# Kernel tuning notes

Hardware: AMD Instinct MI355X
Metric: run time of the kernel (lower is better)

## Reference

```python
import jax, jax.numpy as jnp
import numpy as np

N_IN = 1024
N_OUT = 1024
T, B = 512, 64


def setup_inputs() -> dict:
    key = jax.random.key(0)
    k1, k2, k3, k4, k5 = jax.random.split(key, 5)
    X = jax.random.normal(k1, (T, B, N_IN), dtype=jnp.float32)
    W = jax.random.normal(k2, (N_IN + N_OUT, 4 * N_OUT), dtype=jnp.float32) * 0.02
    b = jax.random.normal(k3, (4 * N_OUT,), dtype=jnp.float32) * 0.02
    y0 = jax.random.normal(k4, (B, N_OUT), dtype=jnp.float32)
    c0 = jax.random.normal(k5, (B, N_OUT), dtype=jnp.float32)
    i = jnp.ones((T, B), dtype=jnp.float32)  # sequence mask
    return {"X": X, "W": W, "b": b, "y0": y0, "c0": c0, "i": i}


def _lstm_low_mem(X, W, b, y0, c0, i):
    H = y0.shape[-1]
    Wx, Wh = W[: X.shape[-1]], W[X.shape[-1]:]
    # precompute input projection for all steps: [T,B,4H]
    Zx = jnp.einsum('tbi,ih->tbh', X, Wx) + b

    def step(carry, inp):
        y_prev, c_prev = carry
        zx_t, m_t = inp
        z = zx_t + y_prev @ Wh  # [B,4H]
        cell_in = jnp.tanh(z[:, :H])
        in_gate = jax.nn.sigmoid(z[:, H:2 * H])
        fgt_gate = jax.nn.sigmoid(z[:, 2 * H:3 * H])
        out_gate = jax.nn.sigmoid(z[:, 3 * H:])
        c = cell_in * in_gate + c_prev * fgt_gate
        y = jnp.tanh(c) * out_gate
        m = m_t[:, None]
        c = m * c + (1.0 - m) * c_prev
        y = m * y
        return (y, c), (y, c)

    (yT, cT), (Y, C) = jax.lax.scan(step, (y0, c0), (Zx, i))
    return Y, C, cT


def reference(X, W, b, y0, c0, i):
    return _lstm_low_mem(X, W, b, y0, c0, i)
```

## Files before the change

### kernel.cpp

```cpp
#include <hip/hip_runtime.h>
#include <cstdint>
#include <cstddef>

#define T_STEPS 512
#define BB 64
#define NIN 1024
#define HB 1024
#define NGC 4096
#define NSCAN 128
#define HC 8
#define WLDH 1032
#define DRING 16

typedef __attribute__((ext_vector_type(8))) short short8;
typedef __attribute__((ext_vector_type(4))) float float4v;
typedef __attribute__((ext_vector_type(2))) float float2v;

__device__ __forceinline__ unsigned short f2bf(float f) {
    union { float f; unsigned u; } v; v.f = f;
    unsigned r = v.u + 0x7fffu + ((v.u >> 16) & 1u);
    return (unsigned short)(r >> 16);
}

union S8U { short8 v; unsigned short u[8]; unsigned w[4]; };

__global__ void __launch_bounds__(256) cvt_y0_kernel(const float* __restrict__ y0,
                                                     unsigned short* __restrict__ yb1) {
    size_t i = ((size_t)blockIdx.x * 256 + threadIdx.x) * 8;
    float4v a = *(const float4v*)(y0 + i);
    float4v b = *(const float4v*)(y0 + i + 4);
    S8U o;
    o.u[0] = f2bf(a[0]); o.u[1] = f2bf(a[1]); o.u[2] = f2bf(a[2]); o.u[3] = f2bf(a[3]);
    o.u[4] = f2bf(b[0]); o.u[5] = f2bf(b[1]); o.u[6] = f2bf(b[2]); o.u[7] = f2bf(b[3]);
    *(short8*)(yb1 + i) = o.v;
}

__global__ void __launch_bounds__(256, 1)
lstm_fused(const float* __restrict__ X, const float* __restrict__ W,
           const float* __restrict__ bias, const float* __restrict__ y0,
           const float* __restrict__ c0, const float* __restrict__ imask,
           float* __restrict__ out, unsigned* __restrict__ prog,
           float* __restrict__ zring)
{
    extern __shared__ char smem[];
    unsigned short* Wl = (unsigned short*)smem;
    float* zl = (float*)(smem + 32 * WLDH * 2);
    float* cl = zl + 64 * 33;
    float* bl = cl + 64 * 8;

    const int bid = blockIdx.x;
    const bool is_scan = bid < NSCAN;
    const int g   = is_scan ? bid : bid - NSCAN;
    const int tid = threadIdx.x;

    {
        const int kbase = is_scan ? NIN : 0;
        for (int task = tid; task < 1024 * 4; task += 256) {
            int k = task >> 2, gt = task & 3;
            const float* src = W + (size_t)(kbase + k) * NGC + (size_t)gt * HB + (size_t)g * HC;
            #pragma unroll
            for (int c = 0; c < 8; ++c)
                Wl[(gt * 8 + c) * WLDH + k] = f2bf(src[c]);
        }
    }
    if (is_scan) {
        if (tid < 32) {
            int gt = tid >> 3, c = tid & 7;
            bl[tid] = bias[gt * HB + g * HC + c];
        }
        for (int p = tid; p < 512; p += 256) {
            int r = p >> 3, c = p & 7;
            cl[r * 8 + c] = c0[(size_t)r * HB + g * HC + c];
        }
    }
    __syncthreads();

    const int w = tid >> 6, l = tid & 63;
    const int m16 = l & 15, q = l >> 4;
    const int arow = w * 16 + m16;
    const int koff = q * 8;
    const unsigned short* wl0 = Wl + (size_t)m16 * WLDH + koff;
    const unsigned short* wl1 = Wl + (size_t)(16 + m16) * WLDH + koff;

    if (!is_scan) {
        unsigned* fslot = prog + NSCAN + g;
        unsigned* sslot = prog + g;
        for (int t = 0; t < T_STEPS; ++t) {
            float4v acc0 = {0.f, 0.f, 0.f, 0.f};
            float4v acc1 = {0.f, 0.f, 0.f, 0.f};
            const float* xs = X + ((size_t)t * BB + arow) * NIN + koff;
            float4v fbv0[4], fbv1[4];
            #pragma unroll
            for (int p = 0; p < 4; ++p) {
                fbv0[p] = *(const float4v*)(xs + p * 32);
                fbv1[p] = *(const float4v*)(xs + p * 32 + 4);
            }
            #pragma unroll
            for (int kb = 0; kb < 32; ++kb) {
                float4v f0 = fbv0[kb & 3], f1 = fbv1[kb & 3];
                if (kb + 4 < 32) {
                    fbv0[kb & 3] = *(const float4v*)(xs + (kb + 4) * 32);
                    fbv1[kb & 3] = *(const float4v*)(xs + (kb + 4) * 32 + 4);
                }
                S8U o;
                o.u[0] = f2bf(f0[0]); o.u[1] = f2bf(f0[1]); o.u[2] = f2bf(f0[2]); o.u[3] = f2bf(f0[3]);
                o.u[4] = f2bf(f1[0]); o.u[5] = f2bf(f1[1]); o.u[6] = f2bf(f1[2]); o.u[7] = f2bf(f1[3]);
                short8 b0 = *(const short8*)(wl0 + kb * 32);
                short8 b1 = *(const short8*)(wl1 + kb * 32);
                acc0 = __builtin_amdgcn_mfma_f32_16x16x32_bf16(o.v, b0, acc0, 0, 0, 0);
                acc1 = __builtin_amdgcn_mfma_f32_16x16x32_bf16(o.v, b1, acc1, 0, 0, 0);
            }
            if (t >= DRING) {
                if (tid == 0) {
                    const unsigned tgt = (unsigned)(t - DRING + 1);
                    unsigned v;
                    while (1) {
                        asm volatile("global_load_dword %0, %1, off sc0 sc1\n\t"
                                     "s_waitcnt vmcnt(0)" : "=v"(v) : "v"(sslot) : "memory");
                        if (v >= tgt) break;
                        __builtin_amdgcn_s_sleep(2);
                    }
                }
                __syncthreads();
            }
            float* zdst = zring + ((size_t)(t % DRING) * NSCAN + g) * 2048;
            #pragma unroll
            for (int i2 = 0; i2 < 4; ++i2) {
                float* p0 = zdst + (size_t)(w * 16 + q * 4 + i2) * 32 + m16;
                asm volatile("global_store_dword %0, %1, off sc0 sc1" :: "v"(p0), "v"(acc0[i2]) : "memory");
                asm volatile("global_store_dword %0, %1, off offset:64 sc0 sc1" :: "v"(p0), "v"(acc1[i2]) : "memory");
            }
            asm volatile("s_waitcnt vmcnt(0)" ::: "memory");
            __syncthreads();
            if (tid == 0) {
                unsigned v = (unsigned)(t + 1);
                asm volatile("global_store_dword %0, %1, off sc0 sc1" :: "v"(fslot), "v"(v) : "memory");
            }
        }
        return;
    }

    float* Yout  = out;
    float* Cout  = out + (size_t)T_STEPS * BB * HB;
    float* cTout = Cout + (size_t)T_STEPS * BB * HB;
    unsigned short* yb0 = (unsigned short*)cTout;
    unsigned short* yb1 = yb0 + BB * HB;

    const int gr = tid >> 2;
    const int gc = (tid & 3) << 1;

    const unsigned* pp0 = prog + l;
    const unsigned* pp1 = prog + 64 + l;
    const unsigned* ppf = prog + NSCAN + g;

    for (int t = 0; t < T_STEPS; ++t) {
        float mrow = imask[(size_t)t * BB + gr];

        if (tid < 64) {
            unsigned a0, a1, ff;
            const unsigned st = (unsigned)t, ft = (unsigned)(t + 1);
            while (1) {
                asm volatile("global_load_dword %0, %1, off sc0 sc1" : "=v"(a0) : "v"(pp0));
                asm volatile("global_load_dword %0, %1, off sc0 sc1" : "=v"(a1) : "v"(pp1));
                asm volatile("global_load_dword %0, %1, off sc0 sc1" : "=v"(ff) : "v"(ppf));
                asm volatile("s_waitcnt vmcnt(0)" ::: "memory");
                bool ok = (a0 >= st) & (a1 >= st) & (ff >= ft);
                if (__ballot(ok) == ~0ull) break;
                __builtin_amdgcn_s_sleep(2);
            }
        }
        __syncthreads();

        const unsigned short* ybr = ((t & 1) ? yb0 : yb1) + (size_t)arow * HB + koff;
        short8 yreg[32];
        #pragma unroll
        for (int kb = 0; kb < 32; ++kb)
            asm volatile("global_load_dwordx4 %0, %1, off offset:%2 sc0 sc1"
                         : "=v"(yreg[kb]) : "v"(ybr), "i"(kb * 64));
        const float* zp = zring + ((size_t)(t % DRING) * NSCAN + g) * 2048 + (size_t)gr * 32 + gc;
        float2v zx0, zx1, zx2, zx3;
        asm volatile("global_load_dwordx2 %0, %1, off sc0 sc1"            : "=v"(zx0) : "v"(zp));
        asm volatile("global_load_dwordx2 %0, %1, off offset:32 sc0 sc1"  : "=v"(zx1) : "v"(zp));
        asm volatile("global_load_dwordx2 %0, %1, off offset:64 sc0 sc1"  : "=v"(zx2) : "v"(zp));
        asm volatile("global_load_dwordx2 %0, %1, off offset:96 sc0 sc1"  : "=v"(zx3) : "v"(zp));

        short8 b0a[4], b1a[4];
        #pragma unroll
        for (int p = 0; p < 4; ++p) {
            b0a[p] = *(const short8*)(wl0 + p * 32);
            b1a[p] = *(const short8*)(wl1 + p * 32);
        }
        asm volatile("s_waitcnt vmcnt(0)" ::: "memory");
        __builtin_amdgcn_sched_barrier(0);

        float4v acc0 = {0.f, 0.f, 0.f, 0.f};
        float4v acc1 = {0.f, 0.f, 0.f, 0.f};
        #pragma unroll
        for (int kb = 0; kb < 32; ++kb) {
            short8 b0 = b0a[kb & 3], b1 = b1a[kb & 3];
            if (kb + 4 < 32) {
                b0a[kb & 3] = *(const short8*)(wl0 + (kb + 4) * 32);
                b1a[kb & 3] = *(const short8*)(wl1 + (kb + 4) * 32);
            }
            acc0 = __builtin_amdgcn_mfma_f32_16x16x32_bf16(yreg[kb], b0, acc0, 0, 0, 0);
            acc1 = __builtin_amdgcn_mfma_f32_16x16x32_bf16(yreg[kb], b1, acc1, 0, 0, 0);
        }

        #pragma unroll
        for (int i2 = 0; i2 < 4; ++i2) {
            int r = w * 16 + q * 4 + i2;
            zl[r * 33 + m16]      = acc0[i2];
            zl[r * 33 + 16 + m16] = acc1[i2];
        }
        __syncthreads();

        if (t == T_STEPS - 1) {
            if (tid == 0) {
                unsigned v = (unsigned)(T_STEPS + 1);
                asm volatile("global_store_dword %0, %1, off sc0 sc1" :: "v"(prog + g), "v"(v) : "memory");
            }
            if (tid < 64) {
                unsigned a0, a1;
                const unsigned st = (unsigned)(T_STEPS + 1);
                while (1) {
                    asm volatile("global_load_dword %0, %1, off sc0 sc1" : "=v"(a0) : "v"(pp0));
                    asm volatile("global_load_dword %0, %1, off sc0 sc1" : "=v"(a1) : "v"(pp1));
                    asm volatile("s_waitcnt vmcnt(0)" ::: "memory");
                    bool ok = (a0 >= st) & (a1 >= st);
                    if (__ballot(ok) == ~0ull) break;
                    __builtin_amdgcn_s_sleep(2);
                }
            }
            __syncthreads();
        }

        {
            const int r = gr, c = gc;
            float z00 = zl[r * 33 + c]      + zx0[0] + bl[c];
            float z01 = zl[r * 33 + c + 1]  + zx0[1] + bl[c + 1];
            float z10 = zl[r * 33 + 8 + c]  + zx1[0] + bl[8 + c];
            float z11 = zl[r * 33 + 9 + c]  + zx1[1] + bl[9 + c];
            float z20 = zl[r * 33 + 16 + c] + zx2[0] + bl[16 + c];
            float z21 = zl[r * 33 + 17 + c] + zx2[1] + bl[17 + c];
            float z30 = zl[r * 33 + 24 + c] + zx3[0] + bl[24 + c];
            float z31 = zl[r * 33 + 25 + c] + zx3[1] + bl[25 + c];
            float cp0 = cl[r * 8 + c], cp1 = cl[r * 8 + c + 1];
            float m = mrow;
            float cell0 = tanhf(z00),                 cell1 = tanhf(z01);
            float ig0 = 1.f / (1.f + __expf(-z10)),   ig1 = 1.f / (1.f + __expf(-z11));
            float fg0 = 1.f / (1.f + __expf(-z20)),   fg1 = 1.f / (1.f + __expf(-z21));
            float og0 = 1.f / (1.f + __expf(-z30)),   og1 = 1.f / (1.f + __expf(-z31));
            float cn0 = cell0 * ig0 + cp0 * fg0,      cn1 = cell1 * ig1 + cp1 * fg1;
            float yn0 = tanhf(cn0) * og0,             yn1 = tanhf(cn1) * og1;
            cn0 = m * cn0 + (1.f - m) * cp0;          cn1 = m * cn1 + (1.f - m) * cp1;
            yn0 *= m;                                 yn1 *= m;
            cl[r * 8 + c] = cn0; cl[r * 8 + c + 1] = cn1;

            if (t < T_STEPS - 1) {
                unsigned short* ybw = ((t & 1) ? yb1 : yb0) + (size_t)r * HB + (size_t)g * HC + c;
                unsigned pk = (unsigned)f2bf(yn0) | ((unsigned)f2bf(yn1) << 16);
                asm volatile("global_store_dword %0, %1, off sc0 sc1" :: "v"(ybw), "v"(pk) : "memory");
                asm volatile("s_waitcnt vmcnt(0)" ::: "memory");
                __syncthreads();
                if (tid == 0) {
                    unsigned v = (unsigned)(t + 1);
                    asm volatile("global_store_dword %0, %1, off sc0 sc1" :: "v"(prog + g), "v"(v) : "memory");
                }
            }

            size_t oidx = ((size_t)t * BB + r) * HB + (size_t)g * HC + c;
            float2v yv = {yn0, yn1}; *(float2v*)(Yout + oidx) = yv;
            float2v cv = {cn0, cn1}; *(float2v*)(Cout + oidx) = cv;
            if (t == T_STEPS - 1) {
                float2v ct = {cn0, cn1};
                *(float2v*)(cTout + (size_t)r * HB + (size_t)g * HC + c) = ct;
            }
        }
    }
}

extern "C" void kernel_launch(void* const* d_in, const int* in_sizes, int n_in,
                              void* d_out, int out_size, void* d_ws, size_t ws_size,
                              hipStream_t stream) {
    const float* X    = (const float*)d_in[0];
    const float* W    = (const float*)d_in[1];
    const float* bias = (const float*)d_in[2];
    const float* y0   = (const float*)d_in[3];
    const float* c0   = (const float*)d_in[4];
    const float* im   = (const float*)d_in[5];
    float* out = (float*)d_out;

    unsigned* prog = (unsigned*)d_ws;
    float* zring   = (float*)((char*)d_ws + 4096);

    unsigned short* yb0 = (unsigned short*)(out + (size_t)2 * T_STEPS * BB * HB);
    unsigned short* yb1 = yb0 + (size_t)BB * HB;

    const int smem_bytes = 32 * WLDH * 2 + 64 * 33 * 4 + 64 * 8 * 4 + 32 * 4;

    hipMemsetAsync(d_ws, 0, 4096, stream);

    cvt_y0_kernel<<<(BB * HB) / (256 * 8), 256, 0, stream>>>(y0, yb1);

    hipFuncSetAttribute((const void*)lstm_fused,
                        hipFuncAttributeMaxDynamicSharedMemorySize, smem_bytes);
    lstm_fused<<<2 * NSCAN, 256, smem_bytes, stream>>>(X, W, bias, y0, c0, im, out, prog, zring);
}
```

Before: 5.337 ms.

## Split recurrent matmul over K across waves with LDS partial-sum reduction

The scan blocks now split the 1024-long K dimension of the recurrent y@Wh product across the four waves, with each wave covering all 64 batch rows over 256 K values, instead of each wave covering 16 rows over the full K. Partial sums go to four separate LDS tiles and are added together in the gate computation. Each wave preloads its weight slice before polling. Each wave now also polls only the 32 producer flags for its own K range, so waiting is spread across the waves and the block-wide barrier before the matmul is dropped. The cost is four times the LDS z-buffer, an extra reduction step, and more registers held live per wave.

```diff
diff --git a/kernel.cpp b/kernel.cpp
--- a/kernel.cpp
+++ b/kernel.cpp
@@ -45,7 +45,7 @@
     extern __shared__ char smem[];
     unsigned short* Wl = (unsigned short*)smem;
     float* zl = (float*)(smem + 32 * WLDH * 2);
-    float* cl = zl + 64 * 33;
+    float* cl = zl + 4 * 64 * 33;
     float* bl = cl + 64 * 8;
 
     const int bid = blockIdx.x;
@@ -77,12 +77,12 @@
 
     const int w = tid >> 6, l = tid & 63;
     const int m16 = l & 15, q = l >> 4;
-    const int arow = w * 16 + m16;
     const int koff = q * 8;
-    const unsigned short* wl0 = Wl + (size_t)m16 * WLDH + koff;
-    const unsigned short* wl1 = Wl + (size_t)(16 + m16) * WLDH + koff;
 
     if (!is_scan) {
+        const unsigned short* wl0 = Wl + (size_t)m16 * WLDH + koff;
+        const unsigned short* wl1 = Wl + (size_t)(16 + m16) * WLDH + koff;
+        const int arow = w * 16 + m16;
         unsigned* fslot = prog + NSCAN + g;
         unsigned* sslot = prog + g;
         for (int t = 0; t < T_STEPS; ++t) {
@@ -146,37 +146,55 @@
     unsigned short* yb0 = (unsigned short*)cTout;
     unsigned short* yb1 = yb0 + BB * HB;
 
+    const int K0 = w * 256;
+    const unsigned short* wlA = Wl + (size_t)m16 * WLDH + K0 + koff;
+    const unsigned short* wlB = Wl + (size_t)(16 + m16) * WLDH + K0 + koff;
+    float* zlw = zl + w * (64 * 33);
+
     const int gr = tid >> 2;
     const int gc = (tid & 3) << 1;
 
+    const unsigned* pollp = prog + 32 * w + (l & 31);
+    const unsigned* ppf   = prog + NSCAN + g;
     const unsigned* pp0 = prog + l;
     const unsigned* pp1 = prog + 64 + l;
-    const unsigned* ppf = prog + NSCAN + g;
 
     for (int t = 0; t < T_STEPS; ++t) {
         float mrow = imask[(size_t)t * BB + gr];
 
-        if (tid < 64) {
-            unsigned a0, a1, ff;
+        short8 bf0[8], bf1[8];
+        #pragma unroll
+        for (int k2 = 0; k2 < 8; ++k2) {
+            bf0[k2] = *(const short8*)(wlA + k2 * 32);
+            bf1[k2] = *(const short8*)(wlB + k2 * 32);
+        }
+
+        {
             const unsigned st = (unsigned)t, ft = (unsigned)(t + 1);
+            unsigned a0, ff;
             while (1) {
-                asm volatile("global_load_dword %0, %1, off sc0 sc1" : "=v"(a0) : "v"(pp0));
-                asm volatile("global_load_dword %0, %1, off sc0 sc1" : "=v"(a1) : "v"(pp1));
+                asm volatile("global_load_dword %0, %1, off sc0 sc1" : "=v"(a0) : "v"(pollp));
                 asm volatile("global_load_dword %0, %1, off sc0 sc1" : "=v"(ff) : "v"(ppf));
                 asm volatile("s_waitcnt vmcnt(0)" ::: "memory");
-                bool ok = (a0 >= st) & (a1 >= st) & (ff >= ft);
+                bool ok = (ff >= ft) && ((l >= 32) || (a0 >= st));
                 if (__ballot(ok) == ~0ull) break;
-                __builtin_amdgcn_s_sleep(2);
-            }
-        }
-        __syncthreads();
-
-        const unsigned short* ybr = ((t & 1) ? yb0 : yb1) + (size_t)arow * HB + koff;
-        short8 yreg[32];
+                __builtin_amdgcn_s_sleep(1);
+            }
+        }
+
+        const unsigned short* ybase = ((t & 1) ? yb0 : yb1);
+        const unsigned short* p0 = ybase + (size_t)m16 * HB + K0 + koff;
+        const unsigned short* p1 = p0 + 16 * HB;
+        const unsigned short* p2 = p0 + 32 * HB;
+        const unsigned short* p3 = p0 + 48 * HB;
+        short8 yA[8], yB[8], yC[8], yD[8];
         #pragma unroll
-        for (int kb = 0; kb < 32; ++kb)
-            asm volatile("global_load_dwordx4 %0, %1, off offset:%2 sc0 sc1"
-                         : "=v"(yreg[kb]) : "v"(ybr), "i"(kb * 64));
+        for (int k2 = 0; k2 < 8; ++k2) {
+            asm volatile("global_load_dwordx4 %0, %1, off offset:%2 sc0 sc1" : "=v"(yA[k2]) : "v"(p0), "i"(k2 * 64));
+            asm volatile("global_load_dwordx4 %0, %1, off offset:%2 sc0 sc1" : "=v"(yB[k2]) : "v"(p1), "i"(k2 * 64));
+            asm volatile("global_load_dwordx4 %0, %1, off offset:%2 sc0 sc1" : "=v"(yC[k2]) : "v"(p2), "i"(k2 * 64));
+            asm volatile("global_load_dwordx4 %0, %1, off offset:%2 sc0 sc1" : "=v"(yD[k2]) : "v"(p3), "i"(k2 * 64));
+        }
         const float* zp = zring + ((size_t)(t % DRING) * NSCAN + g) * 2048 + (size_t)gr * 32 + gc;
         float2v zx0, zx1, zx2, zx3;
         asm volatile("global_load_dwordx2 %0, %1, off sc0 sc1"            : "=v"(zx0) : "v"(zp));
@@ -184,33 +202,36 @@
         asm volatile("global_load_dwordx2 %0, %1, off offset:64 sc0 sc1"  : "=v"(zx2) : "v"(zp));
         asm volatile("global_load_dwordx2 %0, %1, off offset:96 sc0 sc1"  : "=v"(zx3) : "v"(zp));
 
-        short8 b0a[4], b1a[4];
+        asm volatile("s_waitcnt vmcnt(0) lgkmcnt(0)" ::: "memory");
+        __builtin_amdgcn_sched_barrier(0);
+
+        float4v aA0 = {0.f,0.f,0.f,0.f}, aA1 = {0.f,0.f,0.f,0.f};
+        float4v aB0 = {0.f,0.f,0.f,0.f}, aB1 = {0.f,0.f,0.f,0.f};
+        float4v aC0 = {0.f,0.f,0.f,0.f}, aC1 = {0.f,0.f,0.f,0.f};
+        float4v aD0 = {0.f,0.f,0.f,0.f}, aD1 = {0.f,0.f,0.f,0.f};
         #pragma unroll
-        for (int p = 0; p < 4; ++p) {
-            b0a[p] = *(const short8*)(wl0 + p * 32);
-            b1a[p] = *(const short8*)(wl1 + p * 32);
-        }
-        asm volatile("s_waitcnt vmcnt(0)" ::: "memory");
-        __builtin_amdgcn_sched_barrier(0);
-
-        float4v acc0 = {0.f, 0.f, 0.f, 0.f};
-        float4v acc1 = {0.f, 0.f, 0.f, 0.f};
-        #pragma unroll
-        for (int kb = 0; kb < 32; ++kb) {
-            short8 b0 = b0a[kb & 3], b1 = b1a[kb & 3];
-            if (kb + 4 < 32) {
-                b0a[kb & 3] = *(const short8*)(wl0 + (kb + 4) * 32);
-                b1a[kb & 3] = *(const short8*)(wl1 + (kb + 4) * 32);
-            }
-            acc0 = __builtin_amdgcn_mfma_f32_16x16x32_bf16(yreg[kb], b0, acc0, 0, 0, 0);
-            acc1 = __builtin_amdgcn_mfma_f32_16x16x32_bf16(yreg[kb], b1, acc1, 0, 0, 0);
+        for (int k2 = 0; k2 < 8; ++k2) {
+            short8 b0 = bf0[k2], b1 = bf1[k2];
+            aA0 = __builtin_amdgcn_mfma_f32_16x16x32_bf16(yA[k2], b0, aA0, 0, 0, 0);
+            aA1 = __builtin_amdgcn_mfma_f32_16x16x32_bf16(yA[k2], b1, aA1, 0, 0, 0);
+            aB0 = __builtin_amdgcn_mfma_f32_16x16x32_bf16(yB[k2], b0, aB0, 0, 0, 0);
+            aB1 = __builtin_amdgcn_mfma_f32_16x16x32_bf16(yB[k2], b1, aB1, 0, 0, 0);
+            aC0 = __builtin_amdgcn_mfma_f32_16x16x32_bf16(yC[k2], b0, aC0, 0, 0, 0);
+            aC1 = __builtin_amdgcn_mfma_f32_16x16x32_bf16(yC[k2], b1, aC1, 0, 0, 0);
+            aD0 = __builtin_amdgcn_mfma_f32_16x16x32_bf16(yD[k2], b0, aD0, 0, 0, 0);
+            aD1 = __builtin_amdgcn_mfma_f32_16x16x32_bf16(yD[k2], b1, aD1, 0, 0, 0);
         }
 
         #pragma unroll
         for (int i2 = 0; i2 < 4; ++i2) {
-            int r = w * 16 + q * 4 + i2;
-            zl[r * 33 + m16]      = acc0[i2];
-            zl[r * 33 + 16 + m16] = acc1[i2];
+            zlw[( 0 + q * 4 + i2) * 33 + m16]      = aA0[i2];
+            zlw[( 0 + q * 4 + i2) * 33 + 16 + m16] = aA1[i2];
+            zlw[(16 + q * 4 + i2) * 33 + m16]      = aB0[i2];
+            zlw[(16 + q * 4 + i2) * 33 + 16 + m16] = aB1[i2];
+            zlw[(32 + q * 4 + i2) * 33 + m16]      = aC0[i2];
+            zlw[(32 + q * 4 + i2) * 33 + 16 + m16] = aC1[i2];
+            zlw[(48 + q * 4 + i2) * 33 + m16]      = aD0[i2];
+            zlw[(48 + q * 4 + i2) * 33 + 16 + m16] = aD1[i2];
         }
         __syncthreads();
 
@@ -236,14 +257,17 @@
 
         {
             const int r = gr, c = gc;
-            float z00 = zl[r * 33 + c]      + zx0[0] + bl[c];
-            float z01 = zl[r * 33 + c + 1]  + zx0[1] + bl[c + 1];
-            float z10 = zl[r * 33 + 8 + c]  + zx1[0] + bl[8 + c];
-            float z11 = zl[r * 33 + 9 + c]  + zx1[1] + bl[9 + c];
-            float z20 = zl[r * 33 + 16 + c] + zx2[0] + bl[16 + c];
-            float z21 = zl[r * 33 + 17 + c] + zx2[1] + bl[17 + c];
-            float z30 = zl[r * 33 + 24 + c] + zx3[0] + bl[24 + c];
-            float z31 = zl[r * 33 + 25 + c] + zx3[1] + bl[25 + c];
+            const int rb = r * 33;
+            #define ZS(o) (zl[(o)] + zl[2112 + (o)] + zl[4224 + (o)] + zl[6336 + (o)])
+            float z00 = ZS(rb + c)      + zx0[0] + bl[c];
+            float z01 = ZS(rb + c + 1)  + zx0[1] + bl[c + 1];
+            float z10 = ZS(rb + 8 + c)  + zx1[0] + bl[8 + c];
+            float z11 = ZS(rb + 9 + c)  + zx1[1] + bl[9 + c];
+            float z20 = ZS(rb + 16 + c) + zx2[0] + bl[16 + c];
+            float z21 = ZS(rb + 17 + c) + zx2[1] + bl[17 + c];
+            float z30 = ZS(rb + 24 + c) + zx3[0] + bl[24 + c];
+            float z31 = ZS(rb + 25 + c) + zx3[1] + bl[25 + c];
+            #undef ZS
             float cp0 = cl[r * 8 + c], cp1 = cl[r * 8 + c + 1];
             float m = mrow;
             float cell0 = tanhf(z00),                 cell1 = tanhf(z01);
@@ -293,10 +317,9 @@
     unsigned* prog = (unsigned*)d_ws;
     float* zring   = (float*)((char*)d_ws + 4096);
 
-    unsigned short* yb0 = (unsigned short*)(out + (size_t)2 * T_STEPS * BB * HB);
-    unsigned short* yb1 = yb0 + (size_t)BB * HB;
-
-    const int smem_bytes = 32 * WLDH * 2 + 64 * 33 * 4 + 64 * 8 * 4 + 32 * 4;
+    unsigned short* yb1 = (unsigned short*)(out + (size_t)2 * T_STEPS * BB * HB) + (size_t)BB * HB;
+
+    const int smem_bytes = 32 * WLDH * 2 + 4 * 64 * 33 * 4 + 64 * 8 * 4 + 32 * 4;
 
     hipMemsetAsync(d_ws, 0, 4096, stream);
 
```

New measurement: 5.274 ms. No clear change (-1.2%).
